# Optimization experiments

Hardware: AMD Instinct MI355X
Metric: run time of the kernel (lower is better)

The kernel has to match this reference:

```python
import jax, jax.numpy as jnp
import numpy as np

B, S, H, NH = 1, 2048, 2048, 32
HD = H // NH  # 64
DFF = 4 * H
EPS = 1e-5


def layer_norm(x, w, b):
    mu = jnp.mean(x, axis=-1, keepdims=True)
    var = jnp.var(x, axis=-1, keepdims=True)
    return (x - mu) * jax.lax.rsqrt(var + EPS) * w + b


def setup_inputs() -> dict:
    key = jax.random.key(0)
    ks = jax.random.split(key, 16)
    std = 0.02
    hidden_states = jax.random.normal(ks[0], (B, S, H), dtype=jnp.float32)
    # additive causal mask [1,1,S,S]
    causal = jnp.tril(jnp.ones((S, S), dtype=jnp.bool_))
    attention_mask = jnp.where(causal, 0.0, -1e9).astype(jnp.float32)[None, None]
    p = lambda k, shp: (jax.random.normal(k, shp, dtype=jnp.float32) * std)
    return {
        "hidden_states": hidden_states,
        "attention_mask": attention_mask,
        "ln1_w": jnp.ones((H,), jnp.float32), "ln1_b": jnp.zeros((H,), jnp.float32),
        "wq": p(ks[1], (H, H)), "bq": jnp.zeros((H,), jnp.float32),
        "wk": p(ks[2], (H, H)), "bk": jnp.zeros((H,), jnp.float32),
        "wv": p(ks[3], (H, H)), "bv": jnp.zeros((H,), jnp.float32),
        "wo": p(ks[4], (H, H)), "bo": jnp.zeros((H,), jnp.float32),
        "w1": p(ks[5], (H, DFF)), "b1": jnp.zeros((DFF,), jnp.float32),
        "w2": p(ks[6], (DFF, H)), "b2": jnp.zeros((H,), jnp.float32),
        "ln2_w": jnp.ones((H,), jnp.float32), "ln2_b": jnp.zeros((H,), jnp.float32),
    }


def reference(hidden_states, attention_mask, ln1_w, ln1_b, wq, bq, wk, bk, wv, bv,
              wo, bo, w1, b1, w2, b2, ln2_w, ln2_b):
    x = hidden_states
    # --- pre-norm attention ---
    residual = x
    h = layer_norm(x, ln1_w, ln1_b)
    scaling = HD ** -0.5
    q = (h @ wq + bq).reshape(B, S, NH, HD) * scaling
    k = (h @ wk + bk).reshape(B, S, NH, HD)
    v = (h @ wv + bv).reshape(B, S, NH, HD)
    scores = jnp.einsum('bqhd,bkhd->bhqk', q, k) + attention_mask
    p = jax.nn.softmax(scores, axis=-1)  # dropout is identity in eval
    attn = jnp.einsum('bhqk,bkhd->bqhd', p, v).reshape(B, S, H)
    attn = attn @ wo + bo
    x = residual + attn
    # --- pre-norm MLP ---
    residual = x
    h = layer_norm(x, ln2_w, ln2_b)
    h = jax.nn.gelu(h @ w1 + b1, approximate=False) @ w2 + b2
    return residual + h
```

## Files before the change

kernel.cpp:

```cpp
#include <hip/hip_runtime.h>
#include <math.h>

#define H 2048
#define S 2048
#define NH 32
#define HD 64
#define DFF 8192

typedef __attribute__((ext_vector_type(4))) float f32x4;
typedef __attribute__((ext_vector_type(8))) short short8;

static __device__ __forceinline__ ushort f2bf(float f) {
  unsigned u = __float_as_uint(f);
  u += 0x7fff + ((u >> 16) & 1);
  return (ushort)(u >> 16);
}

static __device__ __forceinline__ void gl_lds16(const ushort* g, ushort* l) {
  __builtin_amdgcn_global_load_lds(
      (__attribute__((address_space(1))) const void*)g,
      (__attribute__((address_space(3))) void*)l, 16, 0, 0);
}

__global__ __launch_bounds__(256) void transpose_cast_kernel(
    const float* __restrict__ W, ushort* __restrict__ Wt, int K, int N) {
  __shared__ __align__(16) ushort tile[64][72];
  int n0 = blockIdx.x * 64, k0 = blockIdx.y * 64;
  int t = threadIdx.x;
  int lk = t >> 4;
  int ln4 = (t & 15) * 4;
#pragma unroll
  for (int p = 0; p < 4; p++) {
    int k = p * 16 + lk;
    float4 v = *reinterpret_cast<const float4*>(&W[(size_t)(k0 + k) * N + n0 + ln4]);
    float vv[4] = {v.x, v.y, v.z, v.w};
#pragma unroll
    for (int i = 0; i < 4; i++) {
      int row = ln4 + i;
      int slot = ((k >> 3) ^ (row & 7));
      tile[row][(slot << 3) + (k & 7)] = f2bf(vv[i]);
    }
  }
  __syncthreads();
  int n = t >> 2;
  int kq = (t & 3) * 8;
#pragma unroll
  for (int p = 0; p < 2; p++) {
    int kk = kq + p * 32;
    int slot = ((kk >> 3) ^ (n & 7));
    short8 o = *reinterpret_cast<const short8*>(&tile[n][slot << 3]);
    *reinterpret_cast<short8*>(&Wt[(size_t)(n0 + n) * K + k0 + kk]) = o;
  }
}

__global__ __launch_bounds__(256) void vtrans_kernel(
    const ushort* __restrict__ V, ushort* __restrict__ VT) {
  __shared__ ushort tile[32][33];
  int s0 = blockIdx.x * 32, d0 = blockIdx.y * 32;
  int tx = threadIdx.x & 31, ty = threadIdx.x >> 5;
#pragma unroll
  for (int i = 0; i < 4; i++)
    tile[ty * 4 + i][tx] = V[(size_t)(s0 + ty * 4 + i) * H + d0 + tx];
  __syncthreads();
#pragma unroll
  for (int i = 0; i < 4; i++)
    VT[(size_t)(d0 + ty * 4 + i) * S + s0 + tx] = tile[tx][ty * 4 + i];
}

__global__ __launch_bounds__(256) void biascat_kernel(
    const float* __restrict__ bq, const float* __restrict__ bk,
    const float* __restrict__ bv, float* __restrict__ o) {
  int t = blockIdx.x * 256 + threadIdx.x;
  o[t] = (t < H) ? bq[t] : (t < 2 * H) ? bk[t - H] : bv[t - 2 * H];
}

__global__ __launch_bounds__(256) void ln_kernel(
    const float* __restrict__ x, const float* __restrict__ w,
    const float* __restrict__ b, ushort* __restrict__ out) {
  int row = blockIdx.x, t = threadIdx.x;
  const float4* xr = reinterpret_cast<const float4*>(x + (size_t)row * H);
  float4 v0 = xr[t * 2], v1 = xr[t * 2 + 1];
  float s = v0.x + v0.y + v0.z + v0.w + v1.x + v1.y + v1.z + v1.w;
  float q = v0.x * v0.x + v0.y * v0.y + v0.z * v0.z + v0.w * v0.w +
            v1.x * v1.x + v1.y * v1.y + v1.z * v1.z + v1.w * v1.w;
#pragma unroll
  for (int off = 32; off > 0; off >>= 1) {
    s += __shfl_down(s, off, 64);
    q += __shfl_down(q, off, 64);
  }
  __shared__ float sm[8];
  int lane = t & 63, wv = t >> 6;
  if (lane == 0) { sm[wv] = s; sm[wv + 4] = q; }
  __syncthreads();
  s = sm[0] + sm[1] + sm[2] + sm[3];
  q = sm[4] + sm[5] + sm[6] + sm[7];
  float mu = s * (1.0f / H);
  float var = q * (1.0f / H) - mu * mu;
  float rs = rsqrtf(var + 1e-5f);
  const float4* wr = reinterpret_cast<const float4*>(w);
  const float4* br = reinterpret_cast<const float4*>(b);
  float4 w0 = wr[t * 2], w1v = wr[t * 2 + 1], b0 = br[t * 2], b1v = br[t * 2 + 1];
  short8 pk;
  pk[0] = (short)f2bf((v0.x - mu) * rs * w0.x + b0.x);
  pk[1] = (short)f2bf((v0.y - mu) * rs * w0.y + b0.y);
  pk[2] = (short)f2bf((v0.z - mu) * rs * w0.z + b0.z);
  pk[3] = (short)f2bf((v0.w - mu) * rs * w0.w + b0.w);
  pk[4] = (short)f2bf((v1.x - mu) * rs * w1v.x + b1v.x);
  pk[5] = (short)f2bf((v1.y - mu) * rs * w1v.y + b1v.y);
  pk[6] = (short)f2bf((v1.z - mu) * rs * w1v.z + b1v.z);
  pk[7] = (short)f2bf((v1.w - mu) * rs * w1v.w + b1v.w);
  *reinterpret_cast<short8*>(out + (size_t)row * H + t * 8) = pk;
}

__global__ __launch_bounds__(256) void combine4_kernel(
    const float* __restrict__ res, const float* __restrict__ p0,
    const float* __restrict__ p1, const float* __restrict__ p2,
    const float* __restrict__ p3, const float* __restrict__ bias,
    float* __restrict__ out) {
  size_t i = (size_t)blockIdx.x * 256 + threadIdx.x;
  float4 a = reinterpret_cast<const float4*>(res)[i];
  float4 c0 = reinterpret_cast<const float4*>(p0)[i];
  float4 c1 = reinterpret_cast<const float4*>(p1)[i];
  float4 c2 = reinterpret_cast<const float4*>(p2)[i];
  float4 c3 = reinterpret_cast<const float4*>(p3)[i];
  int col = (int)((i * 4) & (H - 1));
  float4 bb = *reinterpret_cast<const float4*>(bias + col);
  float4 o;
  o.x = a.x + c0.x + c1.x + c2.x + c3.x + bb.x;
  o.y = a.y + c0.y + c1.y + c2.y + c3.y + bb.y;
  o.z = a.z + c0.z + c1.z + c2.z + c3.z + bb.z;
  o.w = a.w + c0.w + c1.w + c2.w + c3.w + bb.w;
  reinterpret_cast<float4*>(out)[i] = o;
}

__global__ __launch_bounds__(256) void combine_ln_kernel(
    const float* __restrict__ res, const float* __restrict__ p0,
    const float* __restrict__ p1, const float* __restrict__ bias,
    const float* __restrict__ lw, const float* __restrict__ lb,
    float* __restrict__ xout, ushort* __restrict__ lnout) {
  int row = blockIdx.x, t = threadIdx.x;
  const float4* rr = reinterpret_cast<const float4*>(res + (size_t)row * H);
  const float4* r0 = reinterpret_cast<const float4*>(p0 + (size_t)row * H);
  const float4* r1 = reinterpret_cast<const float4*>(p1 + (size_t)row * H);
  const float4* bb = reinterpret_cast<const float4*>(bias);
  float4 a0 = rr[t * 2], a1 = rr[t * 2 + 1];
  float4 c0 = r0[t * 2], c1 = r0[t * 2 + 1];
  float4 d0 = r1[t * 2], d1 = r1[t * 2 + 1];
  float4 e0 = bb[t * 2], e1 = bb[t * 2 + 1];
  float4 v0, v1;
  v0.x = a0.x + c0.x + d0.x + e0.x;
  v0.y = a0.y + c0.y + d0.y + e0.y;
  v0.z = a0.z + c0.z + d0.z + e0.z;
  v0.w = a0.w + c0.w + d0.w + e0.w;
  v1.x = a1.x + c1.x + d1.x + e1.x;
  v1.y = a1.y + c1.y + d1.y + e1.y;
  v1.z = a1.z + c1.z + d1.z + e1.z;
  v1.w = a1.w + c1.w + d1.w + e1.w;
  float4* xo = reinterpret_cast<float4*>(xout + (size_t)row * H);
  xo[t * 2] = v0;
  xo[t * 2 + 1] = v1;
  float s = v0.x + v0.y + v0.z + v0.w + v1.x + v1.y + v1.z + v1.w;
  float q = v0.x * v0.x + v0.y * v0.y + v0.z * v0.z + v0.w * v0.w +
            v1.x * v1.x + v1.y * v1.y + v1.z * v1.z + v1.w * v1.w;
#pragma unroll
  for (int off = 32; off > 0; off >>= 1) {
    s += __shfl_down(s, off, 64);
    q += __shfl_down(q, off, 64);
  }
  __shared__ float sm[8];
  int lane = t & 63, wv = t >> 6;
  if (lane == 0) { sm[wv] = s; sm[wv + 4] = q; }
  __syncthreads();
  s = sm[0] + sm[1] + sm[2] + sm[3];
  q = sm[4] + sm[5] + sm[6] + sm[7];
  float mu = s * (1.0f / H);
  float var = q * (1.0f / H) - mu * mu;
  float rs = rsqrtf(var + 1e-5f);
  const float4* wr = reinterpret_cast<const float4*>(lw);
  const float4* br = reinterpret_cast<const float4*>(lb);
  float4 w0 = wr[t * 2], w1v = wr[t * 2 + 1], b0 = br[t * 2], b1v = br[t * 2 + 1];
  short8 pk;
  pk[0] = (short)f2bf((v0.x - mu) * rs * w0.x + b0.x);
  pk[1] = (short)f2bf((v0.y - mu) * rs * w0.y + b0.y);
  pk[2] = (short)f2bf((v0.z - mu) * rs * w0.z + b0.z);
  pk[3] = (short)f2bf((v0.w - mu) * rs * w0.w + b0.w);
  pk[4] = (short)f2bf((v1.x - mu) * rs * w1v.x + b1v.x);
  pk[5] = (short)f2bf((v1.y - mu) * rs * w1v.y + b1v.y);
  pk[6] = (short)f2bf((v1.z - mu) * rs * w1v.z + b1v.z);
  pk[7] = (short)f2bf((v1.w - mu) * rs * w1v.w + b1v.w);
  *reinterpret_cast<short8*>(lnout + (size_t)row * H + t * 8) = pk;
}

template <int MODE>
__global__ __launch_bounds__(512, 2) void gemm256_kernel(
    const ushort* __restrict__ A, const ushort* __restrict__ Bt,
    const float* __restrict__ bias,
    ushort* __restrict__ outb, float* __restrict__ outf,
    int M, int N, int lda, int kbeg, int klen) {
  __shared__ __align__(16) ushort As[2][256 * 64];
  __shared__ __align__(16) ushort Bs[2][256 * 64];
  int tid = threadIdx.x, lane = tid & 63, w = tid >> 6;
  int lm = lane & 15, kg = lane >> 4;
  int wr = w >> 2, wc = w & 3;
  int gx = gridDim.x, nwg = gx * gridDim.y;
  int orig = blockIdx.y * gx + blockIdx.x;
  int wg = (orig & 7) * (nwg >> 3) + (orig >> 3);
  int m0 = (wg % gx) * 256, n0 = (wg / gx) * 256;
  int kb0 = kbeg + blockIdx.z * klen;

  f32x4 acc[8][4] = {};

  const ushort* srcA[4];
  const ushort* srcB[4];
  int dbase[4];
#pragma unroll
  for (int q = 0; q < 4; q++) {
    int g = q * 512 + tid;
    int row = g >> 3, gc = g & 7;
    int col = (gc ^ (row & 7)) << 3;
    srcA[q] = A + (size_t)(m0 + row) * lda + kb0 + col;
    srcB[q] = Bt + (size_t)(n0 + row) * lda + kb0 + col;
    dbase[q] = (q * 512 + w * 64) * 8;
  }

  int nK = klen >> 6;
#pragma unroll
  for (int q = 0; q < 4; q++) gl_lds16(srcA[q], &As[0][dbase[q]]);
#pragma unroll
  for (int q = 0; q < 4; q++) gl_lds16(srcB[q], &Bs[0][dbase[q]]);

  for (int kt = 0; kt < nK; kt++) {
    int cur = kt & 1, nxt = cur ^ 1;
    bool hn = (kt + 1 < nK);
    int ko = (kt + 1) << 6;
    if (hn) {
      gl_lds16(srcA[0] + ko, &As[nxt][dbase[0]]);
      gl_lds16(srcA[1] + ko, &As[nxt][dbase[1]]);
      gl_lds16(srcA[2] + ko, &As[nxt][dbase[2]]);
      gl_lds16(srcA[3] + ko, &As[nxt][dbase[3]]);
      gl_lds16(srcB[0] + ko, &Bs[nxt][dbase[0]]);
      gl_lds16(srcB[1] + ko, &Bs[nxt][dbase[1]]);
      gl_lds16(srcB[2] + ko, &Bs[nxt][dbase[2]]);
      gl_lds16(srcB[3] + ko, &Bs[nxt][dbase[3]]);
      asm volatile("s_waitcnt vmcnt(8)" ::: "memory");
    } else {
      asm volatile("s_waitcnt vmcnt(0)" ::: "memory");
    }
    __builtin_amdgcn_s_barrier();

    short8 bf[4][2], af[4][2], ag[4][2];
#pragma unroll
    for (int n = 0; n < 4; n++)
#pragma unroll
      for (int s = 0; s < 2; s++)
        bf[n][s] = *reinterpret_cast<const short8*>(
            &Bs[cur][(wc * 64 + n * 16 + lm) * 64 + (((s * 4 + kg) ^ (lm & 7)) << 3)]);
#pragma unroll
    for (int i = 0; i < 4; i++)
#pragma unroll
      for (int s = 0; s < 2; s++)
        af[i][s] = *reinterpret_cast<const short8*>(
            &As[cur][(wr * 128 + i * 16 + lm) * 64 + (((s * 4 + kg) ^ (lm & 7)) << 3)]);

    __builtin_amdgcn_s_setprio(1);
#pragma unroll
    for (int i = 0; i < 4; i++)
#pragma unroll
      for (int n = 0; n < 2; n++)
#pragma unroll
        for (int s = 0; s < 2; s++)
          acc[i][n] = __builtin_amdgcn_mfma_f32_16x16x32_bf16(af[i][s], bf[n][s], acc[i][n], 0, 0, 0);
    __builtin_amdgcn_s_setprio(0);

#pragma unroll
    for (int i = 0; i < 4; i++)
#pragma unroll
      for (int s = 0; s < 2; s++)
        ag[i][s] = *reinterpret_cast<const short8*>(
            &As[cur][(wr * 128 + 64 + i * 16 + lm) * 64 + (((s * 4 + kg) ^ (lm & 7)) << 3)]);

    __builtin_amdgcn_s_setprio(1);
#pragma unroll
    for (int i = 0; i < 4; i++)
#pragma unroll
      for (int n = 2; n < 4; n++)
#pragma unroll
        for (int s = 0; s < 2; s++)
          acc[i][n] = __builtin_amdgcn_mfma_f32_16x16x32_bf16(af[i][s], bf[n][s], acc[i][n], 0, 0, 0);
    __builtin_amdgcn_s_setprio(0);

    __builtin_amdgcn_s_setprio(1);
#pragma unroll
    for (int i = 0; i < 4; i++)
#pragma unroll
      for (int n = 0; n < 2; n++)
#pragma unroll
        for (int s = 0; s < 2; s++)
          acc[4 + i][n] = __builtin_amdgcn_mfma_f32_16x16x32_bf16(ag[i][s], bf[n][s], acc[4 + i][n], 0, 0, 0);
    __builtin_amdgcn_s_setprio(0);

    __builtin_amdgcn_s_setprio(1);
#pragma unroll
    for (int i = 0; i < 4; i++)
#pragma unroll
      for (int n = 2; n < 4; n++)
#pragma unroll
        for (int s = 0; s < 2; s++)
          acc[4 + i][n] = __builtin_amdgcn_mfma_f32_16x16x32_bf16(ag[i][s], bf[n][s], acc[4 + i][n], 0, 0, 0);
    __builtin_amdgcn_s_setprio(0);

    __builtin_amdgcn_s_barrier();
  }

#pragma unroll
  for (int mi = 0; mi < 8; mi++) {
#pragma unroll
    for (int ni = 0; ni < 4; ni++) {
#pragma unroll
      for (int r = 0; r < 4; r++) {
        int row = m0 + wr * 128 + mi * 16 + kg * 4 + r;
        int col = n0 + wc * 64 + ni * 16 + lm;
        float v = acc[mi][ni][r];
        if (MODE == 0) {
          float t = v + bias[col];
          float sc = (col < H) ? 0.125f : 1.0f;
          size_t idx = (size_t)(col >> 11) * ((size_t)S * H) + (size_t)row * H + (col & (H - 1));
          outb[idx] = f2bf(t * sc);
        } else if (MODE == 1) {
          float t = v + bias[col];
          outb[(size_t)row * N + col] = f2bf(0.5f * t * (1.0f + erff(t * 0.70710678118f)));
        } else {
          int zs = blockIdx.z + ((blockIdx.z >> 1) << 1);
          outf[(size_t)zs * M * N + (size_t)row * N + col] = v;
        }
      }
    }
  }
}

__global__ __launch_bounds__(512) void attn_kernel(
    const ushort* __restrict__ Q, const ushort* __restrict__ Kmat,
    const ushort* __restrict__ VT, ushort* __restrict__ ctx) {
  __shared__ __align__(16) ushort Ks[2][128 * 64];
  __shared__ __align__(16) ushort Vs[2][64 * 128];
  __shared__ __align__(16) ushort Ps[8 * 16 * 64];
  int h = blockIdx.x;
  int x = blockIdx.y;
  int tid = threadIdx.x, lane = tid & 63, w = tid >> 6;
  int lm = lane & 15, kg = lane >> 4;

  int qbA = x, qbB = 15 - x;
  int tA = x + 1;
  const int nt = 17;

  short8 qa[2];
#pragma unroll
  for (int ks = 0; ks < 2; ks++)
    qa[ks] = *reinterpret_cast<const short8*>(
        Q + (size_t)(qbA * 128 + w * 16 + lm) * H + h * 64 + ks * 32 + kg * 8);

  float m_run[4], l_run[4];
  f32x4 o_acc[4] = {};
#pragma unroll
  for (int r = 0; r < 4; r++) { m_run[r] = -1e30f; l_run[r] = 0.f; }

  auto stage = [&](int kb, int buf) {
#pragma unroll
    for (int p = 0; p < 2; p++) {
      int gbase = p * 512 + w * 64;
      int gran = gbase + lane;
      int krow = gran >> 3, gk = gran & 7;
      gl_lds16(Kmat + (size_t)(kb * 128 + krow) * H + h * 64 + ((gk ^ (krow & 7)) << 3),
               &Ks[buf][gbase * 8]);
    }
#pragma unroll
    for (int p = 0; p < 2; p++) {
      int gbase = p * 512 + w * 64;
      int gran = gbase + lane;
      int vrow = gran >> 4, gv = gran & 15;
      gl_lds16(VT + (size_t)(h * 64 + vrow) * S + kb * 128 + ((gv ^ (vrow & 15)) << 3),
               &Vs[buf][gbase * 8]);
    }
  };

  stage(0, 0);
  __syncthreads();

  for (int t = 0; t < nt; t++) {
    int cur = t & 1;
    if (t + 1 < nt) {
      int tn = t + 1;
      stage((tn < tA) ? tn : tn - tA, cur ^ 1);
    }
    bool diag = (t == tA - 1) || (t == nt - 1);

    f32x4 sacc[8] = {};
#pragma unroll
    for (int j = 0; j < 8; j++) {
      int krow = j * 16 + lm;
#pragma unroll
      for (int ks = 0; ks < 2; ks++) {
        short8 kf = *reinterpret_cast<const short8*>(
            &Ks[cur][krow * 64 + (((ks * 4 + kg) ^ (lm & 7)) << 3)]);
        sacc[j] = __builtin_amdgcn_mfma_f32_16x16x32_bf16(qa[ks], kf, sacc[j], 0, 0, 0);
      }
    }
    if (diag) {
#pragma unroll
      for (int j = 0; j < 8; j++)
#pragma unroll
        for (int r = 0; r < 4; r++)
          if (j * 16 + lm > w * 16 + kg * 4 + r) sacc[j][r] = -1e30f;
    }

#pragma unroll
    for (int r = 0; r < 4; r++) {
      float mx = sacc[0][r];
#pragma unroll
      for (int j = 1; j < 8; j++) mx = fmaxf(mx, sacc[j][r]);
      mx = fmaxf(mx, __shfl_xor(mx, 1, 64));
      mx = fmaxf(mx, __shfl_xor(mx, 2, 64));
      mx = fmaxf(mx, __shfl_xor(mx, 4, 64));
      mx = fmaxf(mx, __shfl_xor(mx, 8, 64));
      float mnew = fmaxf(m_run[r], mx);
      float sc = __expf(m_run[r] - mnew);
      m_run[r] = mnew;
      float ps = 0.f;
#pragma unroll
      for (int j = 0; j < 8; j++) {
        float p = __expf(sacc[j][r] - mnew);
        sacc[j][r] = p;
        ps += p;
      }
      ps += __shfl_xor(ps, 1, 64);
      ps += __shfl_xor(ps, 2, 64);
      ps += __shfl_xor(ps, 4, 64);
      ps += __shfl_xor(ps, 8, 64);
      l_run[r] = l_run[r] * sc + ps;
#pragma unroll
      for (int jd = 0; jd < 4; jd++) o_acc[jd][r] *= sc;
    }

#pragma unroll
    for (int c = 0; c < 2; c++) {
#pragma unroll
      for (int jj = 0; jj < 4; jj++)
#pragma unroll
        for (int r = 0; r < 4; r++) {
          int rl = kg * 4 + r;
          int col = jj * 16 + lm;
          Ps[w * 1024 + rl * 64 + (((col >> 3) ^ (rl & 7)) << 3) + (col & 7)] =
              f2bf(sacc[c * 4 + jj][r]);
        }
      short8 pa[2];
#pragma unroll
      for (int ks = 0; ks < 2; ks++)
        pa[ks] = *reinterpret_cast<const short8*>(
            &Ps[w * 1024 + lm * 64 + (((ks * 4 + kg) ^ (lm & 7)) << 3)]);
#pragma unroll
      for (int jd = 0; jd < 4; jd++) {
        int d = jd * 16 + lm;
#pragma unroll
        for (int ks = 0; ks < 2; ks++) {
          short8 vf = *reinterpret_cast<const short8*>(
              &Vs[cur][d * 128 + (((c * 8 + ks * 4 + kg) ^ lm) << 3)]);
          o_acc[jd] = __builtin_amdgcn_mfma_f32_16x16x32_bf16(pa[ks], vf, o_acc[jd], 0, 0, 0);
        }
      }
    }

    if (t == tA - 1) {
#pragma unroll
      for (int jd = 0; jd < 4; jd++)
#pragma unroll
        for (int r = 0; r < 4; r++)
          ctx[(size_t)(qbA * 128 + w * 16 + kg * 4 + r) * H + h * 64 + jd * 16 + lm] =
              f2bf(o_acc[jd][r] / l_run[r]);
#pragma unroll
      for (int r = 0; r < 4; r++) { m_run[r] = -1e30f; l_run[r] = 0.f; }
#pragma unroll
      for (int jd = 0; jd < 4; jd++) o_acc[jd] = f32x4{0.f, 0.f, 0.f, 0.f};
#pragma unroll
      for (int ks = 0; ks < 2; ks++)
        qa[ks] = *reinterpret_cast<const short8*>(
            Q + (size_t)(qbB * 128 + w * 16 + lm) * H + h * 64 + ks * 32 + kg * 8);
    }
    __syncthreads();
  }

#pragma unroll
  for (int jd = 0; jd < 4; jd++)
#pragma unroll
    for (int r = 0; r < 4; r++)
      ctx[(size_t)(qbB * 128 + w * 16 + kg * 4 + r) * H + h * 64 + jd * 16 + lm] =
          f2bf(o_acc[jd][r] / l_run[r]);
}

extern "C" void kernel_launch(void* const* d_in, const int* in_sizes, int n_in,
                              void* d_out, int out_size, void* d_ws, size_t ws_size,
                              hipStream_t stream) {
  const float* x = (const float*)d_in[0];
  const float* ln1w = (const float*)d_in[2];
  const float* ln1b = (const float*)d_in[3];
  const float* wq = (const float*)d_in[4];
  const float* bq = (const float*)d_in[5];
  const float* wk = (const float*)d_in[6];
  const float* bk = (const float*)d_in[7];
  const float* wv = (const float*)d_in[8];
  const float* bv = (const float*)d_in[9];
  const float* wo = (const float*)d_in[10];
  const float* bo = (const float*)d_in[11];
  const float* w1 = (const float*)d_in[12];
  const float* b1 = (const float*)d_in[13];
  const float* w2 = (const float*)d_in[14];
  const float* b2 = (const float*)d_in[15];
  const float* ln2w = (const float*)d_in[16];
  const float* ln2b = (const float*)d_in[17];
  float* out = (float*)d_out;

  char* ws = (char*)d_ws;
  const size_t MB = 1024 * 1024;
  const size_t SH = (size_t)S * H;
  ushort* WT_QKV = (ushort*)(ws);
  ushort* WT_O = (ushort*)(ws + 24 * MB);
  ushort* WT_1 = (ushort*)(ws + 32 * MB);
  ushort* WT_2 = (ushort*)(ws + 64 * MB);
  ushort* LNO = (ushort*)(ws + 96 * MB);
  ushort* QKVB = (ushort*)(ws + 104 * MB);
  ushort* VTb = (ushort*)(ws + 128 * MB);
  ushort* CTX = (ushort*)(ws + 136 * MB);
  float* X1 = (float*)(ws + 144 * MB);
  float* BIASQ = (float*)(ws + 160 * MB);
  ushort* MID = (ushort*)(ws);
  float* SPA = (float*)(ws + 104 * MB);
  float* SPM = (float*)(ws + 32 * MB);

  transpose_cast_kernel<<<dim3(H / 64, H / 64), 256, 0, stream>>>(wq, WT_QKV, H, H);
  transpose_cast_kernel<<<dim3(H / 64, H / 64), 256, 0, stream>>>(wk, WT_QKV + SH, H, H);
  transpose_cast_kernel<<<dim3(H / 64, H / 64), 256, 0, stream>>>(wv, WT_QKV + 2 * SH, H, H);
  transpose_cast_kernel<<<dim3(H / 64, H / 64), 256, 0, stream>>>(wo, WT_O, H, H);
  transpose_cast_kernel<<<dim3(DFF / 64, H / 64), 256, 0, stream>>>(w1, WT_1, H, DFF);
  transpose_cast_kernel<<<dim3(H / 64, DFF / 64), 256, 0, stream>>>(w2, WT_2, DFF, H);
  biascat_kernel<<<3 * H / 256, 256, 0, stream>>>(bq, bk, bv, BIASQ);

  ln_kernel<<<S, 256, 0, stream>>>(x, ln1w, ln1b, LNO);

  gemm256_kernel<0><<<dim3(S / 256, 3 * H / 256), 512, 0, stream>>>(
      LNO, WT_QKV, BIASQ, QKVB, nullptr, S, 3 * H, H, 0, H);

  vtrans_kernel<<<dim3(S / 32, H / 32), 256, 0, stream>>>(QKVB + 2 * SH, VTb);

  attn_kernel<<<dim3(NH, 8), 512, 0, stream>>>(QKVB, QKVB + SH, VTb, CTX);

  gemm256_kernel<3><<<dim3(S / 256, H / 256, 2), 512, 0, stream>>>(
      CTX, WT_O, nullptr, nullptr, SPA, S, H, H, 0, H / 2);
  combine_ln_kernel<<<S, 256, 0, stream>>>(x, SPA, SPA + SH, bo, ln2w, ln2b, X1, LNO);

  gemm256_kernel<1><<<dim3(S / 256, DFF / 256), 512, 0, stream>>>(
      LNO, WT_1, b1, MID, nullptr, S, DFF, H, 0, H);

  gemm256_kernel<3><<<dim3(S / 256, H / 256, 4), 512, 0, stream>>>(
      MID, WT_2, nullptr, nullptr, SPM, S, H, DFF, 0, DFF / 4);
  combine4_kernel<<<SH / 1024, 256, 0, stream>>>(
      X1, SPM, SPM + SH, SPM + 4 * SH, SPM + 5 * SH, b2, out);
}
```

Measured before the change: 438.6 us.

## Split GEMM k-step into four phases with staggered prefetch and partial waits

Restructures the bf16 MFMA GEMM main loop into four quadrant phases. Each phase reloads only the A/B fragments it needs from LDS and issues a quarter of the next tile's global-to-LDS loads. The load order and vmcnt waits are arranged so that compute on the first A half can start before the second half arrives, and so that the refill is spread across the k-step instead of issued all at once. This adds more barriers per iteration and more LDS fragment reloads, but cuts register pressure and the exposed memory wait.

```diff
diff --git a/kernel.cpp b/kernel.cpp
--- a/kernel.cpp
+++ b/kernel.cpp
@@ -224,92 +224,76 @@
   }
 
   int nK = klen >> 6;
-#pragma unroll
-  for (int q = 0; q < 4; q++) gl_lds16(srcA[q], &As[0][dbase[q]]);
-#pragma unroll
-  for (int q = 0; q < 4; q++) gl_lds16(srcB[q], &Bs[0][dbase[q]]);
+  gl_lds16(srcB[0], &Bs[0][dbase[0]]);
+  gl_lds16(srcB[1], &Bs[0][dbase[1]]);
+  gl_lds16(srcB[2], &Bs[0][dbase[2]]);
+  gl_lds16(srcB[3], &Bs[0][dbase[3]]);
+  gl_lds16(srcA[0], &As[0][dbase[0]]);
+  gl_lds16(srcA[2], &As[0][dbase[2]]);
+  gl_lds16(srcA[1], &As[0][dbase[1]]);
+  gl_lds16(srcA[3], &As[0][dbase[3]]);
+  asm volatile("s_waitcnt vmcnt(2)" ::: "memory");
+  __builtin_amdgcn_s_barrier();
 
   for (int kt = 0; kt < nK; kt++) {
     int cur = kt & 1, nxt = cur ^ 1;
     bool hn = (kt + 1 < nK);
     int ko = (kt + 1) << 6;
-    if (hn) {
-      gl_lds16(srcA[0] + ko, &As[nxt][dbase[0]]);
-      gl_lds16(srcA[1] + ko, &As[nxt][dbase[1]]);
-      gl_lds16(srcA[2] + ko, &As[nxt][dbase[2]]);
-      gl_lds16(srcA[3] + ko, &As[nxt][dbase[3]]);
-      gl_lds16(srcB[0] + ko, &Bs[nxt][dbase[0]]);
-      gl_lds16(srcB[1] + ko, &Bs[nxt][dbase[1]]);
-      gl_lds16(srcB[2] + ko, &Bs[nxt][dbase[2]]);
-      gl_lds16(srcB[3] + ko, &Bs[nxt][dbase[3]]);
-      asm volatile("s_waitcnt vmcnt(8)" ::: "memory");
-    } else {
-      asm volatile("s_waitcnt vmcnt(0)" ::: "memory");
-    }
-    __builtin_amdgcn_s_barrier();
-
-    short8 bf[4][2], af[4][2], ag[4][2];
-#pragma unroll
-    for (int n = 0; n < 4; n++)
-#pragma unroll
-      for (int s = 0; s < 2; s++)
-        bf[n][s] = *reinterpret_cast<const short8*>(
-            &Bs[cur][(wc * 64 + n * 16 + lm) * 64 + (((s * 4 + kg) ^ (lm & 7)) << 3)]);
-#pragma unroll
-    for (int i = 0; i < 4; i++)
-#pragma unroll
-      for (int s = 0; s < 2; s++)
-        af[i][s] = *reinterpret_cast<const short8*>(
-            &As[cur][(wr * 128 + i * 16 + lm) * 64 + (((s * 4 + kg) ^ (lm & 7)) << 3)]);
-
-    __builtin_amdgcn_s_setprio(1);
-#pragma unroll
-    for (int i = 0; i < 4; i++)
+
+    short8 af[4][2], bf[2][2];
+#pragma unroll
+    for (int ph = 0; ph < 4; ph++) {
+      const int mh = ph >> 1, nh = ph & 1;
+#pragma unroll
+      for (int i = 0; i < 4; i++)
+#pragma unroll
+        for (int s = 0; s < 2; s++)
+          af[i][s] = *reinterpret_cast<const short8*>(
+              &As[cur][(wr * 128 + mh * 64 + i * 16 + lm) * 64 +
+                       (((s * 4 + kg) ^ (lm & 7)) << 3)]);
 #pragma unroll
       for (int n = 0; n < 2; n++)
 #pragma unroll
         for (int s = 0; s < 2; s++)
-          acc[i][n] = __builtin_amdgcn_mfma_f32_16x16x32_bf16(af[i][s], bf[n][s], acc[i][n], 0, 0, 0);
-    __builtin_amdgcn_s_setprio(0);
-
-#pragma unroll
-    for (int i = 0; i < 4; i++)
-#pragma unroll
-      for (int s = 0; s < 2; s++)
-        ag[i][s] = *reinterpret_cast<const short8*>(
-            &As[cur][(wr * 128 + 64 + i * 16 + lm) * 64 + (((s * 4 + kg) ^ (lm & 7)) << 3)]);
-
-    __builtin_amdgcn_s_setprio(1);
-#pragma unroll
-    for (int i = 0; i < 4; i++)
-#pragma unroll
-      for (int n = 2; n < 4; n++)
-#pragma unroll
-        for (int s = 0; s < 2; s++)
-          acc[i][n] = __builtin_amdgcn_mfma_f32_16x16x32_bf16(af[i][s], bf[n][s], acc[i][n], 0, 0, 0);
-    __builtin_amdgcn_s_setprio(0);
-
-    __builtin_amdgcn_s_setprio(1);
-#pragma unroll
-    for (int i = 0; i < 4; i++)
-#pragma unroll
-      for (int n = 0; n < 2; n++)
-#pragma unroll
-        for (int s = 0; s < 2; s++)
-          acc[4 + i][n] = __builtin_amdgcn_mfma_f32_16x16x32_bf16(ag[i][s], bf[n][s], acc[4 + i][n], 0, 0, 0);
-    __builtin_amdgcn_s_setprio(0);
-
-    __builtin_amdgcn_s_setprio(1);
-#pragma unroll
-    for (int i = 0; i < 4; i++)
-#pragma unroll
-      for (int n = 2; n < 4; n++)
-#pragma unroll
-        for (int s = 0; s < 2; s++)
-          acc[4 + i][n] = __builtin_amdgcn_mfma_f32_16x16x32_bf16(ag[i][s], bf[n][s], acc[4 + i][n], 0, 0, 0);
-    __builtin_amdgcn_s_setprio(0);
-
-    __builtin_amdgcn_s_barrier();
+          bf[n][s] = *reinterpret_cast<const short8*>(
+              &Bs[cur][(wc * 64 + nh * 32 + n * 16 + lm) * 64 +
+                       (((s * 4 + kg) ^ (lm & 7)) << 3)]);
+      if (hn) {
+        if (ph == 0) {
+          gl_lds16(srcB[0] + ko, &Bs[nxt][dbase[0]]);
+          gl_lds16(srcB[1] + ko, &Bs[nxt][dbase[1]]);
+        } else if (ph == 1) {
+          gl_lds16(srcB[2] + ko, &Bs[nxt][dbase[2]]);
+          gl_lds16(srcB[3] + ko, &Bs[nxt][dbase[3]]);
+        } else if (ph == 2) {
+          gl_lds16(srcA[0] + ko, &As[nxt][dbase[0]]);
+          gl_lds16(srcA[2] + ko, &As[nxt][dbase[2]]);
+        } else {
+          gl_lds16(srcA[1] + ko, &As[nxt][dbase[1]]);
+          gl_lds16(srcA[3] + ko, &As[nxt][dbase[3]]);
+        }
+      }
+      __builtin_amdgcn_s_barrier();
+      asm volatile("s_waitcnt lgkmcnt(0)" ::: "memory");
+      __builtin_amdgcn_sched_barrier(0);
+      __builtin_amdgcn_s_setprio(1);
+#pragma unroll
+      for (int i = 0; i < 4; i++)
+#pragma unroll
+        for (int n = 0; n < 2; n++)
+#pragma unroll
+          for (int s = 0; s < 2; s++)
+            acc[mh * 4 + i][nh * 2 + n] = __builtin_amdgcn_mfma_f32_16x16x32_bf16(
+                af[i][s], bf[n][s], acc[mh * 4 + i][nh * 2 + n], 0, 0, 0);
+      __builtin_amdgcn_s_setprio(0);
+      if (ph == 1) {
+        if (hn) asm volatile("s_waitcnt vmcnt(4)" ::: "memory");
+        else    asm volatile("s_waitcnt vmcnt(0)" ::: "memory");
+      } else if (ph == 3) {
+        if (hn) asm volatile("s_waitcnt vmcnt(2)" ::: "memory");
+      }
+      __builtin_amdgcn_s_barrier();
+    }
   }
 
 #pragma unroll
```

Result: slower. 456.2 us (+4.0%).
